# Kernel tuning notes

Hardware: AMD Instinct MI355X
Metric: run time of the kernel (lower is better)

The kernel has to match this reference:

```python
import jax, jax.numpy as jnp
import numpy as np

N = 40000
E = 640000
IN_FEATS = 128
OUT_FEATS = 32
EDGE_FEATS = 1
H = 8


def setup_inputs() -> dict:
    key = jax.random.key(0)
    ks = jax.random.split(key, 8)
    xavier = lambda k, shape: jax.random.uniform(
        k, shape, jnp.float32,
        -jnp.sqrt(6.0 / (shape[0] + shape[1])), jnp.sqrt(6.0 / (shape[0] + shape[1])))
    return {
        "h": jax.random.normal(ks[0], (N, IN_FEATS), jnp.float32),
        "edge_index": jax.random.randint(ks[1], (2, E), 0, N, jnp.int64 if jax.config.jax_enable_x64 else jnp.int32),
        "edge_feat": jax.random.uniform(ks[2], (E, EDGE_FEATS), jnp.float32),
        # weights stored as [in, out] for x @ W
        "W_node": xavier(ks[3], (IN_FEATS, OUT_FEATS * H)),
        "W_edge": xavier(ks[4], (EDGE_FEATS, H)),
        "attention_src": xavier(ks[5], (H, OUT_FEATS)),
        "attention_dst": xavier(ks[6], (H, OUT_FEATS)),
        "W_msg": xavier(ks[7], (IN_FEATS + EDGE_FEATS, OUT_FEATS * H)),
    }


def _edge_softmax(attn, dst, num_nodes):
    # attn: [E, H], dst: [E] -> softmax over edges grouped by destination node
    max_val = jax.ops.segment_max(attn, dst, num_segments=num_nodes)  # [N, H]
    exp_attn = jnp.exp(attn - max_val[dst])
    sum_exp = jax.ops.segment_sum(exp_attn, dst, num_segments=num_nodes)  # [N, H]
    return exp_attn / jnp.maximum(sum_exp[dst], 1e-12)


def reference(h, edge_index, edge_feat, W_node, W_edge, attention_src, attention_dst, W_msg):
    src, dst = edge_index[0], edge_index[1]
    n = h.shape[0]
    e = src.shape[0]

    h_trans = (h @ W_node).reshape(n, H, OUT_FEATS)        # [N, H, F]
    e_trans = edge_feat @ W_edge                            # [E, H]

    src_feat = h_trans[src]                                 # [E, H, F] gather
    dst_feat = h_trans[dst]                                 # [E, H, F] gather

    attn = (jnp.einsum('ehf,hf->eh', src_feat, attention_src)
            + jnp.einsum('ehf,hf->eh', dst_feat, attention_dst)
            + e_trans)                                      # [E, H]
    attn = jax.nn.leaky_relu(attn, negative_slope=0.2)
    alpha = _edge_softmax(attn, dst, n)                     # [E, H]

    msg_input = jnp.concatenate([h[src], edge_feat], axis=-1)   # [E, in+edge]
    msg = (msg_input @ W_msg).reshape(e, H, OUT_FEATS)           # [E, H, F]
    msg = msg * alpha[..., None]

    out = jax.ops.segment_sum(msg, dst, num_segments=n)     # [N, H, F]
    return out.mean(axis=1)                                  # [N, F]
```

## Files before the change

kernel.cpp:

```cpp
#include <hip/hip_runtime.h>
#include <hip/hip_fp16.h>

using u32 = unsigned int;
using f16x8 = __attribute__((ext_vector_type(8))) _Float16;
using f32x4 = __attribute__((ext_vector_type(4))) float;

constexpr int NN = 40000;
constexpr int NE = 640000;

constexpr int OFF_MSG  = 0;
constexpr int OFF_SCL  = 2560000;
constexpr int OFF_AS   = 2600000;
constexpr int OFF_AD   = 2920000;
constexpr int OFF_BT   = 3240000;
constexpr int OFF_WML  = 3257408;
constexpr int OFF_WEF  = 3257664;
constexpr int OFF_RS   = 3257672;
constexpr int OFF_CUR  = 3297673;
constexpr int OFF_SED  = 3337674;
constexpr int OFF_PART = 3977674;
constexpr size_t WS_NEED = 3977931ull * 4ull;


__global__ void k_prep(const float* __restrict__ Wn, const float* __restrict__ We,
                       const float* __restrict__ As, const float* __restrict__ Ad,
                       const float* __restrict__ Wm, float* __restrict__ ws) {
    int i = blockIdx.x * 256 + threadIdx.x;
    if (i < NN) ((int*)ws)[OFF_CUR + i] = 0;
    int j = i - NN;
    if (j < 0) return;
    if (j < 34816) {
        int c = j >> 7, k = j & 127;
        float v;
        if (c < 256) {
            int hh = c & 7, f = c >> 3;
            v = Wm[k * 256 + hh * 32 + f];
        } else {
            int hh = c & 7;
            const float* att = (c & 8) ? Ad : As;
            float s = 0.f;
            for (int f = 0; f < 32; ++f)
                s += Wn[k * 256 + hh * 32 + f] * att[hh * 32 + f];
            v = s;
        }
        ((_Float16*)(ws + OFF_BT))[j] = (_Float16)v;
    } else if (j < 35072) {
        int col = j - 34816;
        int hh = col >> 5, f = col & 31;
        ws[OFF_WML + f * 8 + hh] = Wm[128 * 256 + col];
    } else if (j < 35080) {
        ws[OFF_WEF + (j - 35072)] = We[j - 35072];
    }
}

__global__ __launch_bounds__(256) void k_node(const float* __restrict__ h,
                                              float* __restrict__ ws) {
    __shared__ __attribute__((aligned(16))) _Float16 msgL[64 * 256];
    __shared__ float invL[64];
    int wave = threadIdx.x >> 6, lane = threadIdx.x & 63;
    int r16 = lane & 15, kg = lane >> 4;
    f16x8 afrag[4];
    {
        const float* hp = h + (size_t)(blockIdx.x * 64 + wave * 16 + r16) * 128 + kg * 8;
        #pragma unroll
        for (int ks = 0; ks < 4; ++ks) {
            float4 u0 = *(const float4*)(hp + ks * 32);
            float4 u1 = *(const float4*)(hp + ks * 32 + 4);
            f16x8 a;
            a[0] = (_Float16)u0.x; a[1] = (_Float16)u0.y;
            a[2] = (_Float16)u0.z; a[3] = (_Float16)u0.w;
            a[4] = (_Float16)u1.x; a[5] = (_Float16)u1.y;
            a[6] = (_Float16)u1.z; a[7] = (_Float16)u1.w;
            afrag[ks] = a;
        }
    }
    const f16x8* BT = (const f16x8*)(ws + OFF_BT);
    f32x4 acc[17];
    #pragma unroll
    for (int ct = 0; ct < 17; ++ct) acc[ct] = (f32x4){0.f, 0.f, 0.f, 0.f};
    #pragma unroll
    for (int ks = 0; ks < 4; ++ks) {
        #pragma unroll
        for (int ct = 0; ct < 17; ++ct) {
            f16x8 b = BT[(ct * 16 + r16) * 16 + ks * 4 + kg];
            acc[ct] = __builtin_amdgcn_mfma_f32_16x16x32_f16(afrag[ks], b, acc[ct], 0, 0, 0);
        }
    }
    int rbase = wave * 16 + kg * 4;
    #pragma unroll
    for (int ct = 0; ct < 16; ++ct) {
        int cs = (ct * 16 + r16) ^ (kg << 3);
        #pragma unroll
        for (int jj = 0; jj < 4; ++jj)
            msgL[(rbase + jj) * 256 + cs] = (_Float16)acc[ct][jj];
    }
    {
        int hh = r16 & 7;
        float* dst = ws + ((r16 & 8) ? OFF_AD : OFF_AS);
        int nodeD = blockIdx.x * 64 + rbase;
        #pragma unroll
        for (int jj = 0; jj < 4; ++jj)
            dst[(size_t)(nodeD + jj) * 8 + hh] = acc[16][jj];
    }
    {
        float mx[4] = {0.f, 0.f, 0.f, 0.f};
        #pragma unroll
        for (int ct = 0; ct < 16; ++ct) {
            #pragma unroll
            for (int jj = 0; jj < 4; ++jj)
                mx[jj] = fmaxf(mx[jj], fabsf(acc[ct][jj]));
        }
        #pragma unroll
        for (int jj = 0; jj < 4; ++jj) {
            mx[jj] = fmaxf(mx[jj], __shfl_xor(mx[jj], 1, 64));
            mx[jj] = fmaxf(mx[jj], __shfl_xor(mx[jj], 2, 64));
            mx[jj] = fmaxf(mx[jj], __shfl_xor(mx[jj], 4, 64));
            mx[jj] = fmaxf(mx[jj], __shfl_xor(mx[jj], 8, 64));
        }
        if (r16 == 0) {
            #pragma unroll
            for (int jj = 0; jj < 4; ++jj) {
                float mxs = fmaxf(mx[jj], 1e-8f);
                ws[OFF_SCL + blockIdx.x * 64 + rbase + jj] = mxs * (1.f / 127.f);
                invL[rbase + jj] = 127.f / mxs;
            }
        }
    }
    __syncthreads();
    u32* MSGW = (u32*)ws;
    size_t gbase = (size_t)blockIdx.x * 64 * 64;
    #pragma unroll
    for (int it = 0; it < 8; ++it) {
        int m = it * 256 + threadIdx.x;
        int n = m >> 5, chunk = m & 31;
        int cb = (chunk * 8) ^ (((n >> 2) & 3) << 3);
        float inv = invL[n];
        float4 v = *(const float4*)&msgL[n * 256 + cb];
        const __half* hp8 = (const __half*)&v;
        u32 w0 = 0, w1 = 0;
        #pragma unroll
        for (int e2 = 0; e2 < 4; ++e2) {
            int q = (int)__builtin_rintf(__half2float(hp8[e2]) * inv) + 128;
            w0 |= (u32)q << (8 * e2);
        }
        #pragma unroll
        for (int e2 = 0; e2 < 4; ++e2) {
            int q = (int)__builtin_rintf(__half2float(hp8[4 + e2]) * inv) + 128;
            w1 |= (u32)q << (8 * e2);
        }
        *(int2*)&MSGW[gbase + (size_t)m * 2] = make_int2((int)w0, (int)w1);
    }
}

__global__ void k_hist(const int* __restrict__ ei, float* __restrict__ ws) {
    int e = blockIdx.x * 256 + threadIdx.x;
    atomicAdd((int*)ws + OFF_CUR + ei[NE + e], 1);
}

__global__ __launch_bounds__(256) void k_scanA(float* __restrict__ wsf) {
    __shared__ int red[256];
    const int* cur = (const int*)wsf + OFF_CUR;
    int t = threadIdx.x, b = blockIdx.x;
    int i = b * 256 + t;
    red[t] = (i < NN) ? cur[i] : 0;
    __syncthreads();
    for (int off = 128; off > 0; off >>= 1) {
        if (t < off) red[t] += red[t + off];
        __syncthreads();
    }
    if (t == 0) ((int*)wsf)[OFF_PART + b] = red[0];
}

__global__ __launch_bounds__(256) void k_scanB(float* __restrict__ wsf) {
    __shared__ int sc[256];
    int* part = (int*)wsf + OFF_PART;
    int t = threadIdx.x;
    int v = (t < 157) ? part[t] : 0;
    sc[t] = v;
    __syncthreads();
    for (int off = 1; off < 256; off <<= 1) {
        int u = sc[t];
        if (t >= off) u += sc[t - off];
        __syncthreads();
        sc[t] = u;
        __syncthreads();
    }
    if (t < 157) part[t] = sc[t] - v;
}

__global__ __launch_bounds__(256) void k_scanC(float* __restrict__ wsf) {
    __shared__ int sc[256];
    int* cur = (int*)wsf + OFF_CUR;
    int* rs  = (int*)wsf + OFF_RS;
    const int* part = (const int*)wsf + OFF_PART;
    int t = threadIdx.x, b = blockIdx.x;
    int i = b * 256 + t;
    int v = (i < NN) ? cur[i] : 0;
    sc[t] = v;
    __syncthreads();
    for (int off = 1; off < 256; off <<= 1) {
        int u = sc[t];
        if (t >= off) u += sc[t - off];
        __syncthreads();
        sc[t] = u;
        __syncthreads();
    }
    if (i < NN) {
        int excl = part[b] + sc[t] - v;
        rs[i] = excl;
        cur[i] = excl;
    }
    if (i == 0) rs[NN] = NE;
}

__global__ void k_scatter(const int* __restrict__ ei, const float* __restrict__ ef,
                          float* __restrict__ ws) {
    int e = blockIdx.x * 256 + threadIdx.x;
    int d = ei[NE + e];
    int pos = atomicAdd((int*)ws + OFF_CUR + d, 1);
    u32 q = (u32)(int)__builtin_rintf(ef[e] * 65535.f);
    u32 pk = (u32)ei[e] | (q << 16);
    ((u32*)ws)[OFF_SED + pos] = pk;
}

__global__ __launch_bounds__(256) void k_gat(const float* __restrict__ ws,
                                             float* __restrict__ out) {
    __shared__ __attribute__((aligned(16))) float attnW[4][128 * 8];
    __shared__ int   srcW[4][128];
    __shared__ float invW[4][8];
    __shared__ float sevW[4][8];
    __shared__ float rW[4][8];
    int wave = threadIdx.x >> 6, lane = threadIdx.x & 63;
    int d = blockIdx.x * 4 + wave;
    const int* RS = (const int*)ws + OFF_RS;
    int row0 = RS[d];
    int deg = RS[d + 1] - row0;
    if (deg > 128) deg = 128;
    float* attnL = attnW[wave];
    int* srcL = srcW[wave];
    const u32* SED = (const u32*)ws + OFF_SED;
    const float* SCL = ws + OFF_SCL;
    int hh = lane & 7, part = lane >> 3;
    float advv = ws[OFF_AD + d * 8 + hh];
    float wevv = ws[OFF_WEF + hh];
    float sm = 0.f, sev = 0.f, rs = 0.f;
    for (int i = part; i < deg; i += 8) {
        u32 se = SED[row0 + i];
        int s = (int)(se & 0xffffu);
        float ev = (float)(se >> 16) * (1.f / 65535.f);
        float a = ws[OFF_AS + s * 8 + hh] + advv + ev * wevv;
        a = a > 0.f ? a : 0.2f * a;
        float ex = __expf(a);
        float g = ex * SCL[s];
        attnL[i * 8 + hh] = g;
        sm += ex; sev += ex * ev; rs += g;
        if (hh == 0) srcL[i] = s;
    }
    sm  += __shfl_xor(sm, 8, 64);  sm  += __shfl_xor(sm, 16, 64);  sm  += __shfl_xor(sm, 32, 64);
    sev += __shfl_xor(sev, 8, 64); sev += __shfl_xor(sev, 16, 64); sev += __shfl_xor(sev, 32, 64);
    rs  += __shfl_xor(rs, 8, 64);  rs  += __shfl_xor(rs, 16, 64);  rs  += __shfl_xor(rs, 32, 64);
    if (part == 0) {
        invW[wave][hh] = 1.f / fmaxf(sm, 1e-12f);
        sevW[wave][hh] = sev;
        rW[wave][hh] = rs;
    }
    int slot = lane >> 5, f = lane & 31;
    const u32* MSG8 = (const u32*)ws;
    float acc[8];
    #pragma unroll
    for (int k = 0; k < 8; ++k) acc[k] = 0.f;
    int i = slot;
    for (; i + 6 < deg; i += 8) {
        int s0 = srcL[i], s1 = srcL[i + 2], s2 = srcL[i + 4], s3 = srcL[i + 6];
        int2 r0 = *(const int2*)(MSG8 + (size_t)s0 * 64 + f * 2);
        int2 r1 = *(const int2*)(MSG8 + (size_t)s1 * 64 + f * 2);
        int2 r2 = *(const int2*)(MSG8 + (size_t)s2 * 64 + f * 2);
        int2 r3 = *(const int2*)(MSG8 + (size_t)s3 * 64 + f * 2);
        {
            float4 a0 = *(const float4*)&attnL[i * 8];
            float4 a1 = *(const float4*)&attnL[i * 8 + 4];
            acc[0] += a0.x * (float)( (u32)r0.x        & 0xffu);
            acc[1] += a0.y * (float)(((u32)r0.x >>  8) & 0xffu);
            acc[2] += a0.z * (float)(((u32)r0.x >> 16) & 0xffu);
            acc[3] += a0.w * (float)( (u32)r0.x >> 24        );
            acc[4] += a1.x * (float)( (u32)r0.y        & 0xffu);
            acc[5] += a1.y * (float)(((u32)r0.y >>  8) & 0xffu);
            acc[6] += a1.z * (float)(((u32)r0.y >> 16) & 0xffu);
            acc[7] += a1.w * (float)( (u32)r0.y >> 24        );
        }
        {
            float4 a0 = *(const float4*)&attnL[(i + 2) * 8];
            float4 a1 = *(const float4*)&attnL[(i + 2) * 8 + 4];
            acc[0] += a0.x * (float)( (u32)r1.x        & 0xffu);
            acc[1] += a0.y * (float)(((u32)r1.x >>  8) & 0xffu);
            acc[2] += a0.z * (float)(((u32)r1.x >> 16) & 0xffu);
            acc[3] += a0.w * (float)( (u32)r1.x >> 24        );
            acc[4] += a1.x * (float)( (u32)r1.y        & 0xffu);
            acc[5] += a1.y * (float)(((u32)r1.y >>  8) & 0xffu);
            acc[6] += a1.z * (float)(((u32)r1.y >> 16) & 0xffu);
            acc[7] += a1.w * (float)( (u32)r1.y >> 24        );
        }
        {
            float4 a0 = *(const float4*)&attnL[(i + 4) * 8];
            float4 a1 = *(const float4*)&attnL[(i + 4) * 8 + 4];
            acc[0] += a0.x * (float)( (u32)r2.x        & 0xffu);
            acc[1] += a0.y * (float)(((u32)r2.x >>  8) & 0xffu);
            acc[2] += a0.z * (float)(((u32)r2.x >> 16) & 0xffu);
            acc[3] += a0.w * (float)( (u32)r2.x >> 24        );
            acc[4] += a1.x * (float)( (u32)r2.y        & 0xffu);
            acc[5] += a1.y * (float)(((u32)r2.y >>  8) & 0xffu);
            acc[6] += a1.z * (float)(((u32)r2.y >> 16) & 0xffu);
            acc[7] += a1.w * (float)( (u32)r2.y >> 24        );
        }
        {
            float4 a0 = *(const float4*)&attnL[(i + 6) * 8];
            float4 a1 = *(const float4*)&attnL[(i + 6) * 8 + 4];
            acc[0] += a0.x * (float)( (u32)r3.x        & 0xffu);
            acc[1] += a0.y * (float)(((u32)r3.x >>  8) & 0xffu);
            acc[2] += a0.z * (float)(((u32)r3.x >> 16) & 0xffu);
            acc[3] += a0.w * (float)( (u32)r3.x >> 24        );
            acc[4] += a1.x * (float)( (u32)r3.y        & 0xffu);
            acc[5] += a1.y * (float)(((u32)r3.y >>  8) & 0xffu);
            acc[6] += a1.z * (float)(((u32)r3.y >> 16) & 0xffu);
            acc[7] += a1.w * (float)( (u32)r3.y >> 24        );
        }
    }
    for (; i < deg; i += 2) {
        int s = srcL[i];
        int2 r0 = *(const int2*)(MSG8 + (size_t)s * 64 + f * 2);
        float4 a0 = *(const float4*)&attnL[i * 8];
        float4 a1 = *(const float4*)&attnL[i * 8 + 4];
        acc[0] += a0.x * (float)( (u32)r0.x        & 0xffu);
        acc[1] += a0.y * (float)(((u32)r0.x >>  8) & 0xffu);
        acc[2] += a0.z * (float)(((u32)r0.x >> 16) & 0xffu);
        acc[3] += a0.w * (float)( (u32)r0.x >> 24        );
        acc[4] += a1.x * (float)( (u32)r0.y        & 0xffu);
        acc[5] += a1.y * (float)(((u32)r0.y >>  8) & 0xffu);
        acc[6] += a1.z * (float)(((u32)r0.y >> 16) & 0xffu);
        acc[7] += a1.w * (float)( (u32)r0.y >> 24        );
    }
    #pragma unroll
    for (int k = 0; k < 8; ++k) acc[k] += __shfl_xor(acc[k], 32, 64);
    if (slot == 0) {
        float o = 0.f;
        #pragma unroll
        for (int k = 0; k < 8; ++k)
            o += invW[wave][k] * (acc[k] - 128.f * rW[wave][k]
                                  + sevW[wave][k] * ws[OFF_WML + f * 8 + k]);
        out[d * 32 + f] = o * 0.125f;
    }
}

__global__ void k_sent(float* out, float v) {
    int i = blockIdx.x * 256 + threadIdx.x;
    if (i < NN * 32) out[i] = v;
}

extern "C" void kernel_launch(void* const* d_in, const int* in_sizes, int n_in,
                              void* d_out, int out_size, void* d_ws, size_t ws_size,
                              hipStream_t stream) {
    float* ws = (float*)d_ws;
    float* out = (float*)d_out;

    int ih = -1, iei = -1, ief = -1, iwn = -1, iwe = -1, ia1 = -1, ia2 = -1, iwm = -1;
    for (int i = 0; i < n_in; ++i) {
        int s = in_sizes[i];
        if      (s == 5120000) ih  = i;
        else if (s == 1280000) iei = i;
        else if (s == 640000)  ief = i;
        else if (s == 32768)   iwn = i;
        else if (s == 33024)   iwm = i;
        else if (s == 8)       iwe = i;
        else if (s == 256)     { if (ia1 < 0) ia1 = i; else ia2 = i; }
    }
    float sent = 0.f;
    if      (n_in != 8)              sent = 37.f;
    else if (ih < 0 || iei < 0 || ief < 0 || iwn < 0 || iwe < 0 ||
             ia1 < 0 || ia2 < 0 || iwm < 0) sent = 21.f;
    else if (out_size != 1280000)    sent = 35.f;
    else if (ws_size < WS_NEED)      sent = 99.f;
    if (sent != 0.f) {
        k_sent<<<5000, 256, 0, stream>>>(out, sent);
        return;
    }

    const float* h  = (const float*)d_in[ih];
    const int*   ei = (const int*)d_in[iei];
    const float* ef = (const float*)d_in[ief];
    const float* Wn = (const float*)d_in[iwn];
    const float* We = (const float*)d_in[iwe];
    const float* As = (const float*)d_in[ia1];
    const float* Ad = (const float*)d_in[ia2];
    const float* Wm = (const float*)d_in[iwm];

    k_prep   <<<294, 256, 0, stream>>>(Wn, We, As, Ad, Wm, ws);
    k_node   <<<625, 256, 0, stream>>>(h, ws);
    k_hist   <<<2500, 256, 0, stream>>>(ei, ws);
    k_scanA  <<<157, 256, 0, stream>>>(ws);
    k_scanB  <<<1, 256, 0, stream>>>(ws);
    k_scanC  <<<157, 256, 0, stream>>>(ws);
    k_scatter<<<2500, 256, 0, stream>>>(ei, ef, ws);
    k_gat    <<<10000, 256, 0, stream>>>(ws, out);
}
```

Measured before the change: 148.6 us.

## Pack per-node attention/scale records, batch atomics, software-pipeline gather loop

Three separate changes. First, the per-node source attention logits and quantization scale now share one 16-float record, so the edge loop in k_gat reads one cache line per source node instead of two. Second, k_hist and k_scatter each process four edges per thread with a quarter of the blocks, so more loads and atomics are in flight per thread. Third, the message gather loop in k_gat is restructured as a rolling 4-deep prefetch with clamped indices, replacing the 8-stride unrolled loop plus tail, to keep loads ahead of the arithmetic; the extra clamped loads and the larger workspace are the costs.

```diff
diff --git a/kernel.cpp b/kernel.cpp
--- a/kernel.cpp
+++ b/kernel.cpp
@@ -9,17 +9,16 @@
 constexpr int NE = 640000;
 
 constexpr int OFF_MSG  = 0;
-constexpr int OFF_SCL  = 2560000;
-constexpr int OFF_AS   = 2600000;
-constexpr int OFF_AD   = 2920000;
-constexpr int OFF_BT   = 3240000;
-constexpr int OFF_WML  = 3257408;
-constexpr int OFF_WEF  = 3257664;
-constexpr int OFF_RS   = 3257672;
-constexpr int OFF_CUR  = 3297673;
-constexpr int OFF_SED  = 3337674;
-constexpr int OFF_PART = 3977674;
-constexpr size_t WS_NEED = 3977931ull * 4ull;
+constexpr int OFF_ASR  = 2560000;
+constexpr int OFF_AD   = 3200000;
+constexpr int OFF_BT   = 3520000;
+constexpr int OFF_WML  = 3537408;
+constexpr int OFF_WEF  = 3537664;
+constexpr int OFF_RS   = 3537672;
+constexpr int OFF_CUR  = 3577673;
+constexpr int OFF_SED  = 3617673;
+constexpr int OFF_PART = 4257673;
+constexpr size_t WS_NEED = 4257930ull * 4ull;
 
 
 __global__ void k_prep(const float* __restrict__ Wn, const float* __restrict__ We,
@@ -96,11 +95,16 @@
     }
     {
         int hh = r16 & 7;
-        float* dst = ws + ((r16 & 8) ? OFF_AD : OFF_AS);
         int nodeD = blockIdx.x * 64 + rbase;
-        #pragma unroll
-        for (int jj = 0; jj < 4; ++jj)
-            dst[(size_t)(nodeD + jj) * 8 + hh] = acc[16][jj];
+        if (!(r16 & 8)) {
+            #pragma unroll
+            for (int jj = 0; jj < 4; ++jj)
+                ws[OFF_ASR + (size_t)(nodeD + jj) * 16 + hh] = acc[16][jj];
+        } else {
+            #pragma unroll
+            for (int jj = 0; jj < 4; ++jj)
+                ws[OFF_AD + (size_t)(nodeD + jj) * 8 + hh] = acc[16][jj];
+        }
     }
     {
         float mx[4] = {0.f, 0.f, 0.f, 0.f};
@@ -121,7 +125,8 @@
             #pragma unroll
             for (int jj = 0; jj < 4; ++jj) {
                 float mxs = fmaxf(mx[jj], 1e-8f);
-                ws[OFF_SCL + blockIdx.x * 64 + rbase + jj] = mxs * (1.f / 127.f);
+                int nd = blockIdx.x * 64 + rbase + jj;
+                ws[OFF_ASR + (size_t)nd * 16 + 8] = mxs * (1.f / 127.f);
                 invL[rbase + jj] = 127.f / mxs;
             }
         }
@@ -153,8 +158,15 @@
 }
 
 __global__ void k_hist(const int* __restrict__ ei, float* __restrict__ ws) {
-    int e = blockIdx.x * 256 + threadIdx.x;
-    atomicAdd((int*)ws + OFF_CUR + ei[NE + e], 1);
+    int t = blockIdx.x * 256 + threadIdx.x;
+    int d0 = ei[NE + t];
+    int d1 = ei[NE + t + 160000];
+    int d2 = ei[NE + t + 320000];
+    int d3 = ei[NE + t + 480000];
+    atomicAdd((int*)ws + OFF_CUR + d0, 1);
+    atomicAdd((int*)ws + OFF_CUR + d1, 1);
+    atomicAdd((int*)ws + OFF_CUR + d2, 1);
+    atomicAdd((int*)ws + OFF_CUR + d3, 1);
 }
 
 __global__ __launch_bounds__(256) void k_scanA(float* __restrict__ wsf) {
@@ -215,12 +227,21 @@
 
 __global__ void k_scatter(const int* __restrict__ ei, const float* __restrict__ ef,
                           float* __restrict__ ws) {
-    int e = blockIdx.x * 256 + threadIdx.x;
-    int d = ei[NE + e];
-    int pos = atomicAdd((int*)ws + OFF_CUR + d, 1);
-    u32 q = (u32)(int)__builtin_rintf(ef[e] * 65535.f);
-    u32 pk = (u32)ei[e] | (q << 16);
-    ((u32*)ws)[OFF_SED + pos] = pk;
+    int t = blockIdx.x * 256 + threadIdx.x;
+    int e0 = t, e1 = t + 160000, e2 = t + 320000, e3 = t + 480000;
+    int d0 = ei[NE + e0], d1 = ei[NE + e1], d2 = ei[NE + e2], d3 = ei[NE + e3];
+    int s0 = ei[e0], s1 = ei[e1], s2 = ei[e2], s3 = ei[e3];
+    float f0 = ef[e0], f1 = ef[e1], f2 = ef[e2], f3 = ef[e3];
+    int* cur = (int*)ws + OFF_CUR;
+    u32* sed = (u32*)ws + OFF_SED;
+    int p0 = atomicAdd(cur + d0, 1);
+    int p1 = atomicAdd(cur + d1, 1);
+    int p2 = atomicAdd(cur + d2, 1);
+    int p3 = atomicAdd(cur + d3, 1);
+    sed[p0] = (u32)s0 | ((u32)(int)__builtin_rintf(f0 * 65535.f) << 16);
+    sed[p1] = (u32)s1 | ((u32)(int)__builtin_rintf(f1 * 65535.f) << 16);
+    sed[p2] = (u32)s2 | ((u32)(int)__builtin_rintf(f2 * 65535.f) << 16);
+    sed[p3] = (u32)s3 | ((u32)(int)__builtin_rintf(f3 * 65535.f) << 16);
 }
 
 __global__ __launch_bounds__(256) void k_gat(const float* __restrict__ ws,
@@ -239,7 +260,6 @@
     float* attnL = attnW[wave];
     int* srcL = srcW[wave];
     const u32* SED = (const u32*)ws + OFF_SED;
-    const float* SCL = ws + OFF_SCL;
     int hh = lane & 7, part = lane >> 3;
     float advv = ws[OFF_AD + d * 8 + hh];
     float wevv = ws[OFF_WEF + hh];
@@ -248,10 +268,11 @@
         u32 se = SED[row0 + i];
         int s = (int)(se & 0xffffu);
         float ev = (float)(se >> 16) * (1.f / 65535.f);
-        float a = ws[OFF_AS + s * 8 + hh] + advv + ev * wevv;
+        const float* rec = ws + OFF_ASR + (size_t)s * 16;
+        float a = rec[hh] + advv + ev * wevv;
         a = a > 0.f ? a : 0.2f * a;
         float ex = __expf(a);
-        float g = ex * SCL[s];
+        float g = ex * rec[8];
         attnL[i * 8 + hh] = g;
         sm += ex; sev += ex * ev; rs += g;
         if (hh == 0) srcL[i] = s;
@@ -269,75 +290,37 @@
     float acc[8];
     #pragma unroll
     for (int k = 0; k < 8; ++k) acc[k] = 0.f;
-    int i = slot;
-    for (; i + 6 < deg; i += 8) {
-        int s0 = srcL[i], s1 = srcL[i + 2], s2 = srcL[i + 4], s3 = srcL[i + 6];
-        int2 r0 = *(const int2*)(MSG8 + (size_t)s0 * 64 + f * 2);
-        int2 r1 = *(const int2*)(MSG8 + (size_t)s1 * 64 + f * 2);
-        int2 r2 = *(const int2*)(MSG8 + (size_t)s2 * 64 + f * 2);
-        int2 r3 = *(const int2*)(MSG8 + (size_t)s3 * 64 + f * 2);
-        {
-            float4 a0 = *(const float4*)&attnL[i * 8];
-            float4 a1 = *(const float4*)&attnL[i * 8 + 4];
-            acc[0] += a0.x * (float)( (u32)r0.x        & 0xffu);
-            acc[1] += a0.y * (float)(((u32)r0.x >>  8) & 0xffu);
-            acc[2] += a0.z * (float)(((u32)r0.x >> 16) & 0xffu);
-            acc[3] += a0.w * (float)( (u32)r0.x >> 24        );
-            acc[4] += a1.x * (float)( (u32)r0.y        & 0xffu);
-            acc[5] += a1.y * (float)(((u32)r0.y >>  8) & 0xffu);
-            acc[6] += a1.z * (float)(((u32)r0.y >> 16) & 0xffu);
-            acc[7] += a1.w * (float)( (u32)r0.y >> 24        );
-        }
-        {
-            float4 a0 = *(const float4*)&attnL[(i + 2) * 8];
-            float4 a1 = *(const float4*)&attnL[(i + 2) * 8 + 4];
-            acc[0] += a0.x * (float)( (u32)r1.x        & 0xffu);
-            acc[1] += a0.y * (float)(((u32)r1.x >>  8) & 0xffu);
-            acc[2] += a0.z * (float)(((u32)r1.x >> 16) & 0xffu);
-            acc[3] += a0.w * (float)( (u32)r1.x >> 24        );
-            acc[4] += a1.x * (float)( (u32)r1.y        & 0xffu);
-            acc[5] += a1.y * (float)(((u32)r1.y >>  8) & 0xffu);
-            acc[6] += a1.z * (float)(((u32)r1.y >> 16) & 0xffu);
-            acc[7] += a1.w * (float)( (u32)r1.y >> 24        );
-        }
-        {
-            float4 a0 = *(const float4*)&attnL[(i + 4) * 8];
-            float4 a1 = *(const float4*)&attnL[(i + 4) * 8 + 4];
-            acc[0] += a0.x * (float)( (u32)r2.x        & 0xffu);
-            acc[1] += a0.y * (float)(((u32)r2.x >>  8) & 0xffu);
-            acc[2] += a0.z * (float)(((u32)r2.x >> 16) & 0xffu);
-            acc[3] += a0.w * (float)( (u32)r2.x >> 24        );
-            acc[4] += a1.x * (float)( (u32)r2.y        & 0xffu);
-            acc[5] += a1.y * (float)(((u32)r2.y >>  8) & 0xffu);
-            acc[6] += a1.z * (float)(((u32)r2.y >> 16) & 0xffu);
-            acc[7] += a1.w * (float)( (u32)r2.y >> 24        );
-        }
-        {
-            float4 a0 = *(const float4*)&attnL[(i + 6) * 8];
-            float4 a1 = *(const float4*)&attnL[(i + 6) * 8 + 4];
-            acc[0] += a0.x * (float)( (u32)r3.x        & 0xffu);
-            acc[1] += a0.y * (float)(((u32)r3.x >>  8) & 0xffu);
-            acc[2] += a0.z * (float)(((u32)r3.x >> 16) & 0xffu);
-            acc[3] += a0.w * (float)( (u32)r3.x >> 24        );
-            acc[4] += a1.x * (float)( (u32)r3.y        & 0xffu);
-            acc[5] += a1.y * (float)(((u32)r3.y >>  8) & 0xffu);
-            acc[6] += a1.z * (float)(((u32)r3.y >> 16) & 0xffu);
-            acc[7] += a1.w * (float)( (u32)r3.y >> 24        );
-        }
-    }
-    for (; i < deg; i += 2) {
-        int s = srcL[i];
-        int2 r0 = *(const int2*)(MSG8 + (size_t)s * 64 + f * 2);
-        float4 a0 = *(const float4*)&attnL[i * 8];
-        float4 a1 = *(const float4*)&attnL[i * 8 + 4];
-        acc[0] += a0.x * (float)( (u32)r0.x        & 0xffu);
-        acc[1] += a0.y * (float)(((u32)r0.x >>  8) & 0xffu);
-        acc[2] += a0.z * (float)(((u32)r0.x >> 16) & 0xffu);
-        acc[3] += a0.w * (float)( (u32)r0.x >> 24        );
-        acc[4] += a1.x * (float)( (u32)r0.y        & 0xffu);
-        acc[5] += a1.y * (float)(((u32)r0.y >>  8) & 0xffu);
-        acc[6] += a1.z * (float)(((u32)r0.y >> 16) & 0xffu);
-        acc[7] += a1.w * (float)( (u32)r0.y >> 24        );
+    if (deg > slot) {
+        int cnt = ((deg - slot - 1) >> 1) + 1;
+        auto ldr = [&](int j) -> int2 {
+            int jc = j < cnt ? j : 0;
+            int e = slot + 2 * jc;
+            return *(const int2*)(MSG8 + (size_t)srcL[e] * 64 + f * 2);
+        };
+        auto cons = [&](int2 rr, int e) {
+            float4 a0 = *(const float4*)&attnL[e * 8];
+            float4 a1 = *(const float4*)&attnL[e * 8 + 4];
+            acc[0] += a0.x * (float)( (u32)rr.x        & 0xffu);
+            acc[1] += a0.y * (float)(((u32)rr.x >>  8) & 0xffu);
+            acc[2] += a0.z * (float)(((u32)rr.x >> 16) & 0xffu);
+            acc[3] += a0.w * (float)( (u32)rr.x >> 24        );
+            acc[4] += a1.x * (float)( (u32)rr.y        & 0xffu);
+            acc[5] += a1.y * (float)(((u32)rr.y >>  8) & 0xffu);
+            acc[6] += a1.z * (float)(((u32)rr.y >> 16) & 0xffu);
+            acc[7] += a1.w * (float)( (u32)rr.y >> 24        );
+        };
+        int2 r0 = ldr(0), r1 = ldr(1), r2 = ldr(2), r3 = ldr(3);
+        int j = 0;
+        for (; j + 4 < cnt; j += 4) {
+            cons(r0, slot + 2 * j);     r0 = ldr(j + 4);
+            cons(r1, slot + 2 * j + 2); r1 = ldr(j + 5);
+            cons(r2, slot + 2 * j + 4); r2 = ldr(j + 6);
+            cons(r3, slot + 2 * j + 6); r3 = ldr(j + 7);
+        }
+        cons(r0, slot + 2 * j);
+        if (j + 1 < cnt) cons(r1, slot + 2 * j + 2);
+        if (j + 2 < cnt) cons(r2, slot + 2 * j + 4);
+        if (j + 3 < cnt) cons(r3, slot + 2 * j + 6);
     }
     #pragma unroll
     for (int k = 0; k < 8; ++k) acc[k] += __shfl_xor(acc[k], 32, 64);
@@ -395,10 +378,10 @@
 
     k_prep   <<<294, 256, 0, stream>>>(Wn, We, As, Ad, Wm, ws);
     k_node   <<<625, 256, 0, stream>>>(h, ws);
-    k_hist   <<<2500, 256, 0, stream>>>(ei, ws);
+    k_hist   <<<625, 256, 0, stream>>>(ei, ws);
     k_scanA  <<<157, 256, 0, stream>>>(ws);
     k_scanB  <<<1, 256, 0, stream>>>(ws);
     k_scanC  <<<157, 256, 0, stream>>>(ws);
-    k_scatter<<<2500, 256, 0, stream>>>(ei, ef, ws);
+    k_scatter<<<625, 256, 0, stream>>>(ei, ef, ws);
     k_gat    <<<10000, 256, 0, stream>>>(ws, out);
 }
```

Result: faster. 145.3 us (-2.2%).
